# Kernel optimization log

Hardware: AMD Instinct MI355X
Metric: run time of the kernel (lower is better)

Reference implementation:

```python
import jax, jax.numpy as jnp
import numpy as np

B, T, D = 4, 4096, 1024
EPS = 1e-6


def setup_inputs() -> dict:
    key = jax.random.key(0)
    ks = jax.random.split(key, 9)
    s = 0.02  # init scale for weights
    f32 = jnp.float32
    return {
        "x_seq": jax.random.normal(ks[0], (B, T, D), f32),
        "W_q": jax.random.normal(ks[1], (D, D), f32) * s,
        "b_q": jax.random.normal(ks[2], (D,), f32) * s,
        "W_k": jax.random.normal(ks[3], (D, D), f32) * s,
        "b_k": jax.random.normal(ks[4], (D,), f32) * s,
        "W_v": jax.random.normal(ks[5], (D, D), f32) * s,
        "b_v": jax.random.normal(ks[6], (D,), f32) * s,
        "W_a": jax.random.normal(ks[7], (D, D), f32) * s,
        "b_a": jax.random.normal(ks[8], (D,), f32) * s,
    }


def reference(x_seq, W_q, b_q, W_k, b_k, W_v, b_v, W_a, b_a):
    # torch nn.Linear: y = x @ W.T + b
    q = jax.nn.relu(x_seq @ W_q.T + b_q)          # [B,T,D]
    k = jax.nn.relu(x_seq @ W_k.T + b_k)          # [B,T,D]
    v = x_seq @ W_v.T + b_v                        # [B,T,D]
    A = jax.nn.sigmoid(x_seq @ W_a.T + b_a)       # [B,T,D]

    # cumprod_A[b,s,i] = prod_{u>=s} A[b,u,i], via reverse cumsum of logs
    log_g = jax.lax.cumsum(jnp.log(A + 1e-6), axis=1, reverse=True)
    wk = k * jnp.exp(log_g)                        # weighted_k [B,T,D]

    # num[b,t,j] = q_t . S_t[:,j] with S_t = cumsum_{s<=t} (wk_s outer v_s)
    # == causal-masked (q @ wk^T) @ v  (same math, no [B,T,D,D] blowup)
    scores = jnp.einsum('btd,bsd->bts', q, wk)     # [B,T,T]
    Tn = x_seq.shape[1]
    mask = jnp.tril(jnp.ones((Tn, Tn), bool))
    scores = jnp.where(mask, scores, 0.0)

    num = jnp.einsum('bts,bsd->btd', scores, v)    # [B,T,D]
    denom = scores.sum(-1, keepdims=True) + EPS    # q_t . Z_t, [B,T,1]
    return num / denom
```

## Files before the change

kernel.cpp:

```cpp
#include <hip/hip_runtime.h>

typedef unsigned short u16;
typedef unsigned int u32;

typedef __bf16 bf16x8 __attribute__((ext_vector_type(8)));
typedef float f32x4 __attribute__((ext_vector_type(4)));
typedef u16 u16x8 __attribute__((ext_vector_type(8)));

#define TSEQ 4096
#define DDIM 1024
#define NB 4
#define EPSV 1e-6f
#define CPITCH 136
#define EPITCH 264

__device__ __forceinline__ u16 f2b(float f) {
    union { float f; u32 u; } v; v.f = f;
    u32 r = v.u + 0x7FFFu + ((v.u >> 16) & 1u);
    return (u16)(r >> 16);
}
__device__ __forceinline__ float b2f(u16 h) {
    union { u32 u; float f; } v; v.u = ((u32)h) << 16; return v.f;
}
__device__ __forceinline__ u16 f2h(float f) {
    union { _Float16 h; u16 u; } v; v.h = (_Float16)f; return v.u;
}
__device__ __forceinline__ float h2f(u16 u) {
    union { u16 u; _Float16 h; } v; v.u = u; return (float)v.h;
}

__global__ __launch_bounds__(256) void k_prep(
    const float* __restrict__ x,
    const float* __restrict__ wq, const float* __restrict__ wk,
    const float* __restrict__ wv, const float* __restrict__ wa,
    const float* __restrict__ bq, const float* __restrict__ bk,
    const float* __restrict__ bv, const float* __restrict__ ba,
    u16* __restrict__ xw, u16* __restrict__ wcat, float* __restrict__ bcat,
    float* __restrict__ denom) {
    int bid = blockIdx.x, tid = threadIdx.x;
    if (bid < 1024) {
        size_t base = (size_t)bid * 4096 + tid;
#pragma unroll
        for (int k = 0; k < 16; ++k) {
            size_t f4 = base + k * 256;
            float4 f = ((const float4*)x)[f4];
            ushort4 u;
            u.x = f2b(f.x); u.y = f2b(f.y); u.z = f2b(f.z); u.w = f2b(f.w);
            *(ushort4*)(xw + f4 * 4) = u;
        }
    } else if (bid < 1280) {
        size_t base = (size_t)(bid - 1024) * 4096 + tid;
#pragma unroll
        for (int k = 0; k < 16; ++k) {
            size_t f4 = base + k * 256;
            int sel = (int)(f4 >> 18);
            const float* src = (sel == 0) ? wq : (sel == 1) ? wk : (sel == 2) ? wv : wa;
            float4 f = ((const float4*)src)[f4 & 262143];
            ushort4 u;
            u.x = f2b(f.x); u.y = f2b(f.y); u.z = f2b(f.z); u.w = f2b(f.w);
            *(ushort4*)(wcat + f4 * 4) = u;
        }
    } else if (bid == 1280) {
#pragma unroll
        for (int c = 0; c < 16; ++c) {
            int j = c * 256 + tid;
            int sel = j >> 10;
            const float* src = (sel == 0) ? bq : (sel == 1) ? bk : (sel == 2) ? bv : ba;
            bcat[j] = src[j & 1023];
        }
    } else {
        float4 z = {0.f, 0.f, 0.f, 0.f};
#pragma unroll
        for (int k = 0; k < 16; ++k)
            ((float4*)denom)[k * 256 + tid] = z;
    }
}

__device__ __forceinline__ void stage_k(u16* __restrict__ dst, const char* __restrict__ base,
                                        int ld2, int kbyte, int wid, int lane) {
#pragma unroll
    for (int c = 0; c < 4; ++c) {
        const char* g = base + c * 8 * ld2 + kbyte;
        char* l = (char*)dst + (wid * 32 + c * 8) * 128 + lane * 16;
        __builtin_amdgcn_global_load_lds((const __attribute__((address_space(1))) u32*)g,
                                         (__attribute__((address_space(3))) u32*)l, 16, 0, 0);
    }
}

__device__ __forceinline__ void mma_tile(const u16* __restrict__ As, const u16* __restrict__ Bs,
                                         f32x4 acc[4][4], int wm, int wn, int quad, int l15) {
#pragma unroll
    for (int kk = 0; kk < 64; kk += 32) {
        int cg = (kk >> 3) + quad;
        bf16x8 a[4], b[4];
#pragma unroll
        for (int i = 0; i < 4; ++i) {
            int arow = wm * 64 + i * 16 + l15;
            int brow = wn * 64 + i * 16 + l15;
            a[i] = *(const bf16x8*)(As + arow * 64 + ((cg ^ (arow & 7)) << 3));
            b[i] = *(const bf16x8*)(Bs + brow * 64 + ((cg ^ (brow & 7)) << 3));
        }
#pragma unroll
        for (int i = 0; i < 4; ++i)
#pragma unroll
            for (int j = 0; j < 4; ++j)
                acc[i][j] = __builtin_amdgcn_mfma_f32_16x16x32_bf16(a[i], b[j], acc[i][j], 0, 0, 0);
    }
}

#define STG_A(dst_d, dst_h, kofs) do { \
    const char* _g = gAt + ((dst_h) * 262144 + wid * 32768 + (kofs)); \
    char* _l = lA + ((dst_d) * 32768 + (dst_h) * 16384); \
    __builtin_amdgcn_global_load_lds((const __attribute__((address_space(1))) u32*)_g, \
        (__attribute__((address_space(3))) u32*)_l, 16, 0, 0); \
    __builtin_amdgcn_global_load_lds((const __attribute__((address_space(1))) u32*)(_g + 16384), \
        (__attribute__((address_space(3))) u32*)(_l + 1024), 16, 0, 0); \
  } while (0)

#define STG_B(dst_d, dst_h, kofs) do { \
    const char* _g = gBt + ((dst_h) * 262144 + wid * 32768 + (kofs)); \
    char* _l = lB + ((dst_d) * 32768 + (dst_h) * 16384); \
    __builtin_amdgcn_global_load_lds((const __attribute__((address_space(1))) u32*)_g, \
        (__attribute__((address_space(3))) u32*)_l, 16, 0, 0); \
    __builtin_amdgcn_global_load_lds((const __attribute__((address_space(1))) u32*)(_g + 16384), \
        (__attribute__((address_space(3))) u32*)(_l + 1024), 16, 0, 0); \
  } while (0)

#define NOP_ ((void)0)
#define VM0_ asm volatile("s_waitcnt vmcnt(0)" ::: "memory")
#define VM4_ asm volatile("s_waitcnt vmcnt(4)" ::: "memory")
#define BAR_ __builtin_amdgcn_s_barrier()
#define LGK_ asm volatile("s_waitcnt lgkmcnt(0)" ::: "memory")
#define SB0_ __builtin_amdgcn_sched_barrier(0)

#define LDA(hh, dd) do { \
    _Pragma("unroll") \
    for (int _i = 0; _i < 4; ++_i) { \
      Ar[_i][0] = *(const bf16x8*)(pA0 + ((dd) * 16384 + (hh) * 8192 + _i * 1024)); \
      Ar[_i][1] = *(const bf16x8*)(pA1 + ((dd) * 16384 + (hh) * 8192 + _i * 1024)); \
    } } while (0)

#define LDB(hh, dd) do { \
    _Pragma("unroll") \
    for (int _j = 0; _j < 2; ++_j) { \
      Br[hh][_j][0] = *(const bf16x8*)(pB0 + ((dd) * 16384 + (hh) * 8192 + _j * 1024)); \
      Br[hh][_j][1] = *(const bf16x8*)(pB1 + ((dd) * 16384 + (hh) * 8192 + _j * 1024)); \
    } } while (0)

#define MMA(qa, qb) do { \
    __builtin_amdgcn_s_setprio(1); \
    _Pragma("unroll") \
    for (int _kk = 0; _kk < 2; ++_kk) \
      _Pragma("unroll") \
      for (int _i = 0; _i < 4; ++_i) \
        _Pragma("unroll") \
        for (int _j = 0; _j < 2; ++_j) \
          acc[(qa) * 4 + _i][(qb) * 2 + _j] = __builtin_amdgcn_mfma_f32_16x16x32_bf16( \
              Ar[_i][_kk], Br[qb][_j][_kk], acc[(qa) * 4 + _i][(qb) * 2 + _j], 0, 0, 0); \
    __builtin_amdgcn_s_setprio(0); \
  } while (0)

__global__ __launch_bounds__(512, 2) void k_gemm_qkva(
    const u16* __restrict__ xw, const u16* __restrict__ wcat, const float* __restrict__ bcat,
    u16* __restrict__ qb, u16* __restrict__ kb, u16* __restrict__ vT, u16* __restrict__ gA,
    float* __restrict__ part) {
    __shared__ __align__(16) char smem[131072];
    u16* As = (u16*)smem;
    u16* Bs = (u16*)(smem + 65536);
    int tid = threadIdx.x;
    int wid = tid >> 6, lane = tid & 63;
    int wm = wid >> 2, wn = wid & 3;
    int quad = lane >> 4, l15 = lane & 15;
    int g8 = lane >> 3, hx = (lane & 7) ^ g8;
    size_t m0 = (size_t)blockIdx.x * 256, n0 = (size_t)blockIdx.y * 256;
    const char* gAp = (const char*)xw + (m0 + g8) * 2048 + hx * 16;
    const char* gBp = (const char*)wcat + (n0 + g8) * 2048 + hx * 16;
    char* lA = smem + wid * 2048 + lane * 16;
    char* lB = smem + 65536 + wid * 2048 + lane * 16;

    int x0 = (quad ^ (l15 & 7)) << 3;
    int x1 = ((quad + 4) ^ (l15 & 7)) << 3;
    const u16* pA0 = As + (wm * 64 + l15) * 64 + x0;
    const u16* pA1 = As + (wm * 64 + l15) * 64 + x1;
    const u16* pB0 = Bs + (wn * 32 + l15) * 64 + x0;
    const u16* pB1 = Bs + (wn * 32 + l15) * 64 + x1;

    f32x4 acc[8][4] = {};
    bf16x8 Ar[4][2];
    bf16x8 Br[2][2][2];

    const char* gAt = gAp;
    const char* gBt = gBp;

    STG_A(0, 0, 0); STG_B(0, 0, 0);
    STG_A(0, 1, 0); STG_B(0, 1, 0);
    STG_A(1, 0, 128); STG_B(1, 0, 128);
    VM4_;
    BAR_;

#pragma unroll 2
    for (int t = 0; t < 14; ++t) {
        int d = t & 1, dn = d ^ 1;
        LDA(0, d); LDB(0, d); LDB(1, d);
        STG_A(dn, 1, 128); STG_B(dn, 1, 128);
        BAR_; LGK_; SB0_; MMA(0, 0); MMA(0, 1); BAR_;
        LDA(1, d);
        STG_A(d, 0, 256); STG_B(d, 0, 256);
        BAR_; LGK_; SB0_; MMA(1, 0); MMA(1, 1); VM4_; BAR_;
        gAt += 128; gBt += 128;
    }
    {
        LDA(0, 0); LDB(0, 0); LDB(1, 0);
        STG_A(1, 1, 128); STG_B(1, 1, 128);
        BAR_; LGK_; SB0_; MMA(0, 0); MMA(0, 1); BAR_;
        LDA(1, 0);
        BAR_; LGK_; SB0_; MMA(1, 0); MMA(1, 1); VM0_; BAR_;
    }
    {
        LDA(0, 1); LDB(0, 1); LDB(1, 1);
        BAR_; LGK_; SB0_; MMA(0, 0); MMA(0, 1); BAR_;
        LDA(1, 1);
        BAR_; LGK_; SB0_; MMA(1, 0); MMA(1, 1); BAR_;
    }

    int blk = (int)(n0 >> 10), nf0 = (int)(n0 & 1023);
    int bB = (int)(m0 >> 12), t0m = (int)(m0 & 4095);
    float bias[4];
#pragma unroll
    for (int j = 0; j < 4; ++j)
        bias[j] = bcat[n0 + (size_t)((j >> 1) * 128 + wn * 32 + (j & 1) * 16 + l15)];
    u16* Cs = (u16*)smem;

#pragma unroll
    for (int h = 0; h < 2; ++h) {
        if (h) __syncthreads();
#pragma unroll
        for (int j = 0; j < 4; ++j) {
            float cs = 0.f;
            int col = (j >> 1) * 128 + wn * 32 + (j & 1) * 16 + l15;
#pragma unroll
            for (int i4 = 0; i4 < 4; ++i4) {
#pragma unroll
                for (int r = 0; r < 4; ++r) {
                    float z = acc[h * 4 + i4][j][r] + bias[j];
                    u16 o;
                    if (blk < 2) {
                        o = f2b(fmaxf(z, 0.f));
                    } else if (blk == 2) {
                        o = f2b(z);
                    } else {
                        float gg = __logf(1.f / (1.f + __expf(-z)) + 1e-6f);
                        o = f2h(gg);
                        cs += gg;
                    }
                    Cs[(wm * 64 + i4 * 16 + quad * 4 + r) * EPITCH + col] = o;
                }
            }
            if (blk == 3) {
                cs += __shfl_xor(cs, 16, 64);
                cs += __shfl_xor(cs, 32, 64);
                if (quad == 0) {
                    int chunk = (t0m >> 6) + h * 2 + wm;
                    part[((size_t)(bB * 64 + chunk) << 10) + nf0 + col] = cs;
                }
            }
        }
        __syncthreads();
        if (blk != 2) {
            u16* dst = (blk == 0) ? qb : (blk == 1) ? kb : gA;
            int lr = tid >> 2, c0 = (tid & 3) * 64;
            size_t rowo = (size_t)(m0 + h * 128 + lr) * 1024 + nf0 + c0;
#pragma unroll
            for (int i = 0; i < 8; ++i)
                *(u16x8*)(dst + rowo + i * 8) = *(const u16x8*)(Cs + lr * EPITCH + c0 + i * 8);
        } else {
            int jc = tid >> 1, th = (tid & 1) * 64;
            size_t rowo = (((size_t)(bB * 1024 + nf0 + jc)) << 12) + t0m + h * 128 + th;
#pragma unroll
            for (int i = 0; i < 8; ++i) {
                u16x8 vv;
#pragma unroll
                for (int e = 0; e < 8; ++e)
                    vv[e] = Cs[(th + i * 8 + e) * EPITCH + jc];
                *(u16x8*)(vT + rowo + i * 8) = vv;
            }
        }
    }
}

__global__ __launch_bounds__(256) void k_scan_apply(
    const u16* __restrict__ gA, const float* __restrict__ part, u16* __restrict__ kb) {
    int c = blockIdx.x, b = blockIdx.y;
    int col = blockIdx.z * 256 + threadIdx.x;
    float r = 0.f;
    for (int c2 = c + 1; c2 < 64; ++c2)
        r += part[((size_t)(b * 64 + c2) << 10) + col];
    size_t base = (((size_t)(b * TSEQ + c * 64)) << 10) + col;
#pragma unroll 4
    for (int s = 63; s >= 0; --s) {
        size_t ro = base + ((size_t)s << 10);
        r += h2f(gA[ro]);
        kb[ro] = f2b(b2f(kb[ro]) * __expf(r));
    }
}

__global__ __launch_bounds__(256) void k_scores(
    const u16* __restrict__ qb, const u16* __restrict__ wkb,
    u16* __restrict__ scores, float* __restrict__ denom) {
    int bid = blockIdx.x, b = blockIdx.y;
    int xc = bid & 7, idx = bid >> 3;
    int rs0 = xc, rs1 = 15 - xc, rs2 = 16 + xc, rs3 = 31 - xc;
    int si = 0, rem = idx;
    for (; si < 32; ++si) {
        int n = (rs0 >= si) + (rs1 >= si) + (rs2 >= si) + (rs3 >= si);
        if (rem < n) break;
        rem -= n;
    }
    int ti = rs3, cnt = 0;
    if (rs0 >= si) { if (cnt == rem) ti = rs0; ++cnt; }
    if (rs1 >= si) { if (cnt == rem) ti = rs1; ++cnt; }
    if (rs2 >= si) { if (cnt == rem) ti = rs2; ++cnt; }
    if (rs3 >= si) { if (cnt == rem) ti = rs3; ++cnt; }
    __shared__ __align__(16) char smem[CPITCH * 128 * 2];
    u16* As = (u16*)smem;
    u16* Bs = (u16*)(smem + 16384);
    int tid = threadIdx.x;
    const u16* A = qb + ((size_t)b << 22);
    const u16* Bm = wkb + ((size_t)b << 22);
    int t0 = ti * 128, s0 = si * 128;
    int wid = tid >> 6, lane = tid & 63;
    int wm = wid >> 1, wn = wid & 1, quad = lane >> 4, l15 = lane & 15;
    int hxor = (lane & 7) ^ (lane >> 3);
    const char* baA = (const char*)A + (size_t)(t0 + wid * 32 + (lane >> 3)) * 2048 + hxor * 16;
    const char* baB = (const char*)Bm + (size_t)(s0 + wid * 32 + (lane >> 3)) * 2048 + hxor * 16;
    f32x4 acc[4][4] = {};
#pragma unroll
    for (int k0 = 0; k0 < DDIM; k0 += 64) {
        stage_k(As, baA, 2048, k0 * 2, wid, lane);
        stage_k(Bs, baB, 2048, k0 * 2, wid, lane);
        __syncthreads();
        mma_tile(As, Bs, acc, wm, wn, quad, l15);
        __syncthreads();
    }
    u16* Cs = (u16*)smem;
#pragma unroll
    for (int im = 0; im < 4; ++im) {
#pragma unroll
        for (int r = 0; r < 4; ++r) {
            int trow = t0 + wm * 64 + im * 16 + quad * 4 + r;
            float rs = 0.f;
#pragma unroll
            for (int jn = 0; jn < 4; ++jn) {
                int s = s0 + wn * 64 + jn * 16 + l15;
                float val = acc[im][jn][r];
                if (s > trow) val = 0.f;
                rs += val;
                Cs[(wm * 64 + im * 16 + quad * 4 + r) * CPITCH + wn * 64 + jn * 16 + l15] = f2b(val);
            }
#pragma unroll
            for (int m = 1; m < 16; m <<= 1) rs += __shfl_xor(rs, m, 64);
            if (l15 == 0) atomicAdd(denom + (b << 12) + trow, rs);
        }
    }
    __syncthreads();
    int r = tid >> 1, ch = (tid & 1) * 64;
    size_t rowo = ((size_t)(b * TSEQ + t0 + r) << 12) + s0 + ch;
#pragma unroll
    for (int i = 0; i < 8; ++i)
        *(u16x8*)(scores + rowo + i * 8) = *(const u16x8*)(Cs + r * CPITCH + ch + i * 8);
}

__global__ __launch_bounds__(256) void k_num(
    const u16* __restrict__ scores, const u16* __restrict__ vT,
    const float* __restrict__ denom, float* __restrict__ out) {
    int ji = blockIdx.x, ti = 31 - blockIdx.y, b = blockIdx.z;
    __shared__ __align__(16) u16 As[128 * 64];
    __shared__ __align__(16) u16 Bs[128 * 64];
    int tid = threadIdx.x;
    const u16* A = scores + ((size_t)b << 24);
    const u16* Bm = vT + ((size_t)b << 22);
    int t0 = ti * 128, j0 = ji * 128;
    int wid = tid >> 6, lane = tid & 63;
    int wm = wid >> 1, wn = wid & 1, quad = lane >> 4, l15 = lane & 15;
    int hxor = (lane & 7) ^ (lane >> 3);
    const char* pA = (const char*)A + (size_t)(t0 + wid * 32 + (lane >> 3)) * 8192 + hxor * 16;
    const char* pB = (const char*)Bm + (size_t)(j0 + wid * 32 + (lane >> 3)) * 8192 + hxor * 16;
    f32x4 acc[4][4] = {};
    int kmax = (ti + 1) * 128;
    for (int k0 = 0; k0 < kmax; k0 += 128) {
        stage_k(As, pA, 8192, 0, wid, lane);
        stage_k(Bs, pB, 8192, 0, wid, lane);
        __syncthreads();
        mma_tile(As, Bs, acc, wm, wn, quad, l15);
        __syncthreads();
        stage_k(As, pA, 8192, 128, wid, lane);
        stage_k(Bs, pB, 8192, 128, wid, lane);
        __syncthreads();
        mma_tile(As, Bs, acc, wm, wn, quad, l15);
        __syncthreads();
        pA += 256; pB += 256;
    }
#pragma unroll
    for (int im = 0; im < 4; ++im) {
#pragma unroll
        for (int r = 0; r < 4; ++r) {
            int t = t0 + wm * 64 + im * 16 + quad * 4 + r;
            float den = denom[(b << 12) + t] + EPSV;
#pragma unroll
            for (int jn = 0; jn < 4; ++jn) {
                int j = j0 + wn * 64 + jn * 16 + l15;
                out[((size_t)(b * TSEQ + t) << 10) + j] = acc[im][jn][r] / den;
            }
        }
    }
}

static const size_t OFF_Q      = 0;
static const size_t OFF_WK     = 33554432;
static const size_t OFF_VT     = 67108864;
static const size_t OFF_DENOM  = 100663296;
static const size_t OFF_BCAT   = 100728832;
static const size_t OFF_XW     = 100745216;
static const size_t OFF_WCAT   = 134299648;
static const size_t OFF_GA     = 176242688;
static const size_t OFF_PART   = 243351552;
static const size_t OFF_SCORES = OFF_XW;

extern "C" void kernel_launch(void* const* d_in, const int* in_sizes, int n_in,
                              void* d_out, int out_size, void* d_ws, size_t ws_size,
                              hipStream_t stream) {
    const float* x  = (const float*)d_in[0];
    const float* Wq = (const float*)d_in[1];
    const float* bq = (const float*)d_in[2];
    const float* Wk = (const float*)d_in[3];
    const float* bk = (const float*)d_in[4];
    const float* Wv = (const float*)d_in[5];
    const float* bv = (const float*)d_in[6];
    const float* Wa = (const float*)d_in[7];
    const float* ba = (const float*)d_in[8];
    float* out = (float*)d_out;

    char* W = (char*)d_ws;
    u16* qb      = (u16*)(W + OFF_Q);
    u16* wkb     = (u16*)(W + OFF_WK);
    u16* vT      = (u16*)(W + OFF_VT);
    float* denom = (float*)(W + OFF_DENOM);
    float* bcat  = (float*)(W + OFF_BCAT);
    u16* xw      = (u16*)(W + OFF_XW);
    u16* wcat    = (u16*)(W + OFF_WCAT);
    u16* gA      = (u16*)(W + OFF_GA);
    float* part  = (float*)(W + OFF_PART);
    u16* scores  = (u16*)(W + OFF_SCORES);

    k_prep<<<1282, 256, 0, stream>>>(x, Wq, Wk, Wv, Wa, bq, bk, bv, ba, xw, wcat, bcat, denom);

    k_gemm_qkva<<<dim3(64, 16), 512, 0, stream>>>(xw, wcat, bcat, qb, wkb, vT, gA, part);

    k_scan_apply<<<dim3(64, NB, 4), 256, 0, stream>>>(gA, part, wkb);

    k_scores<<<dim3(528, NB), 256, 0, stream>>>(qb, wkb, scores, denom);

    k_num<<<dim3(8, 32, NB), 256, 0, stream>>>(scores, vT, denom, out);
}
```

Baseline: 549.7 us.

## Double-buffer LDS tiles in scores and num GEMM kernels

```diff
diff --git a/kernel.cpp b/kernel.cpp
--- a/kernel.cpp
+++ b/kernel.cpp
@@ -107,6 +107,9 @@
                 acc[i][j] = __builtin_amdgcn_mfma_f32_16x16x32_bf16(a[i], b[j], acc[i][j], 0, 0, 0);
     }
 }
+
+#define KVM0_ asm volatile("s_waitcnt vmcnt(0)" ::: "memory")
+#define KBAR_ __builtin_amdgcn_s_barrier()
 
 #define STG_A(dst_d, dst_h, kofs) do { \
     const char* _g = gAt + ((dst_h) * 262144 + wid * 32768 + (kofs)); \
@@ -321,9 +324,9 @@
     if (rs1 >= si) { if (cnt == rem) ti = rs1; ++cnt; }
     if (rs2 >= si) { if (cnt == rem) ti = rs2; ++cnt; }
     if (rs3 >= si) { if (cnt == rem) ti = rs3; ++cnt; }
-    __shared__ __align__(16) char smem[CPITCH * 128 * 2];
+    __shared__ __align__(16) char smem[65536];
     u16* As = (u16*)smem;
-    u16* Bs = (u16*)(smem + 16384);
+    u16* Bs = (u16*)(smem + 32768);
     int tid = threadIdx.x;
     const u16* A = qb + ((size_t)b << 22);
     const u16* Bm = wkb + ((size_t)b << 22);
@@ -334,13 +337,18 @@
     const char* baA = (const char*)A + (size_t)(t0 + wid * 32 + (lane >> 3)) * 2048 + hxor * 16;
     const char* baB = (const char*)Bm + (size_t)(s0 + wid * 32 + (lane >> 3)) * 2048 + hxor * 16;
     f32x4 acc[4][4] = {};
-#pragma unroll
-    for (int k0 = 0; k0 < DDIM; k0 += 64) {
-        stage_k(As, baA, 2048, k0 * 2, wid, lane);
-        stage_k(Bs, baB, 2048, k0 * 2, wid, lane);
-        __syncthreads();
-        mma_tile(As, Bs, acc, wm, wn, quad, l15);
-        __syncthreads();
+    stage_k(As, baA, 2048, 0, wid, lane);
+    stage_k(Bs, baB, 2048, 0, wid, lane);
+    KVM0_; KBAR_;
+#pragma unroll 2
+    for (int t = 0; t < 16; ++t) {
+        int cur = t & 1;
+        if (t < 15) {
+            stage_k(As + (cur ^ 1) * 8192, baA, 2048, (t + 1) * 128, wid, lane);
+            stage_k(Bs + (cur ^ 1) * 8192, baB, 2048, (t + 1) * 128, wid, lane);
+        }
+        mma_tile(As + cur * 8192, Bs + cur * 8192, acc, wm, wn, quad, l15);
+        KVM0_; KBAR_;
     }
     u16* Cs = (u16*)smem;
 #pragma unroll
@@ -374,8 +382,9 @@
     const u16* __restrict__ scores, const u16* __restrict__ vT,
     const float* __restrict__ denom, float* __restrict__ out) {
     int ji = blockIdx.x, ti = 31 - blockIdx.y, b = blockIdx.z;
-    __shared__ __align__(16) u16 As[128 * 64];
-    __shared__ __align__(16) u16 Bs[128 * 64];
+    __shared__ __align__(16) char smem[65536];
+    u16* As = (u16*)smem;
+    u16* Bs = (u16*)(smem + 32768);
     int tid = threadIdx.x;
     const u16* A = scores + ((size_t)b << 24);
     const u16* Bm = vT + ((size_t)b << 22);
@@ -386,19 +395,18 @@
     const char* pA = (const char*)A + (size_t)(t0 + wid * 32 + (lane >> 3)) * 8192 + hxor * 16;
     const char* pB = (const char*)Bm + (size_t)(j0 + wid * 32 + (lane >> 3)) * 8192 + hxor * 16;
     f32x4 acc[4][4] = {};
-    int kmax = (ti + 1) * 128;
-    for (int k0 = 0; k0 < kmax; k0 += 128) {
-        stage_k(As, pA, 8192, 0, wid, lane);
-        stage_k(Bs, pB, 8192, 0, wid, lane);
-        __syncthreads();
-        mma_tile(As, Bs, acc, wm, wn, quad, l15);
-        __syncthreads();
-        stage_k(As, pA, 8192, 128, wid, lane);
-        stage_k(Bs, pB, 8192, 128, wid, lane);
-        __syncthreads();
-        mma_tile(As, Bs, acc, wm, wn, quad, l15);
-        __syncthreads();
-        pA += 256; pB += 256;
+    int nt = (ti + 1) * 2;
+    stage_k(As, pA, 8192, 0, wid, lane);
+    stage_k(Bs, pB, 8192, 0, wid, lane);
+    KVM0_; KBAR_;
+    for (int t = 0; t < nt; ++t) {
+        int cur = t & 1;
+        if (t + 1 < nt) {
+            stage_k(As + (cur ^ 1) * 8192, pA, 8192, (t + 1) * 128, wid, lane);
+            stage_k(Bs + (cur ^ 1) * 8192, pB, 8192, (t + 1) * 128, wid, lane);
+        }
+        mma_tile(As + cur * 8192, Bs + cur * 8192, acc, wm, wn, quad, l15);
+        KVM0_; KBAR_;
     }
 #pragma unroll
     for (int im = 0; im < 4; ++im) {
```

New measurement: 541.5 us. No clear change (-1.5%).
